# Kernel optimization log

Hardware: AMD Instinct MI355X
Metric: run time of the kernel (lower is better)

## Reference

```python
import jax, jax.numpy as jnp
import numpy as np

IN_DIM, MEM_DIM, NUM_WORDS, N_LEAVES = 300, 256, 50000, 8192


def setup_inputs() -> dict:
    key = jax.random.key(0)
    ks = jax.random.split(key, 6)
    s = 0.05
    return {
        "embs": jax.random.normal(ks[0], (N_LEAVES, IN_DIM), jnp.float32),
        "Wx": jax.random.normal(ks[1], (4 * MEM_DIM, IN_DIM), jnp.float32) * s,
        "bx": jax.random.normal(ks[2], (4 * MEM_DIM,), jnp.float32) * s,
        "Wl": jax.random.normal(ks[3], (5 * MEM_DIM, MEM_DIM), jnp.float32) * s,
        "Wr": jax.random.normal(ks[4], (5 * MEM_DIM, MEM_DIM), jnp.float32) * s,
        "emb_table": jax.random.normal(ks[5], (NUM_WORDS, IN_DIM), jnp.float32),
    }


def reference(embs, Wx, bx, Wl, Wr, emb_table):
    m = Wl.shape[1]

    # x-projection order along fused axis: [cx, ix, fx, ox]
    def proj_x(x):  # [B, in] -> [B, 4, m]
        return (x @ Wx.T + bx).reshape(x.shape[0], 4, m)

    # hidden-projection order: [u, i, lf, rf, o]
    def compose(xg, lc, lh, rc, rh):
        lg = (lh @ Wl.T).reshape(-1, 5, m)
        rg = (rh @ Wr.T).reshape(-1, 5, m)
        u = jnp.tanh(xg[:, 0] + lg[:, 0] + rg[:, 0])
        i = jax.nn.sigmoid(xg[:, 1] + lg[:, 1] + rg[:, 1])
        lf = jax.nn.sigmoid(xg[:, 2] + lg[:, 2] + rg[:, 2])  # fx shared
        rf = jax.nn.sigmoid(xg[:, 2] + lg[:, 3] + rg[:, 3])  # fx shared
        c = i * u + lf * lc + rf * rc
        o = jax.nn.sigmoid(xg[:, 3] + lg[:, 4] + rg[:, 4])
        h = o * jnp.tanh(c)
        return c, h

    # leaves: zero child states, per-leaf embedding inputs
    L = embs.shape[0]
    z = jnp.zeros((L, m), embs.dtype)
    c, h = compose(proj_x(embs), z, z, z, z)

    # internal nodes (PAD=True): input is word_embedding(num_words - 1)
    pad_xg = proj_x(emb_table[-1:])  # [1, 4, m]

    while c.shape[0] > 1:  # static shapes; 13 merge levels
        lc, rc = c[0::2], c[1::2]
        lh, rh = h[0::2], h[1::2]
        B = lc.shape[0]
        c, h = compose(jnp.broadcast_to(pad_xg, (B, 4, m)), lc, lh, rc, rh)

    return jnp.stack([c, h])  # root (c, h): [2, 1, mem_dim]
```

## Files before the change

### kernel.cpp

```cpp
#include <hip/hip_runtime.h>
#include <math.h>


#define MEM 256

typedef __attribute__((ext_vector_type(8))) short bf16x8;
typedef __attribute__((ext_vector_type(4))) float f32x4;

__device__ __forceinline__ float sigf(float x) { return 1.0f / (1.0f + __expf(-x)); }

__device__ __forceinline__ unsigned short f2b(float f) {
  unsigned int u = __float_as_uint(f);
  u = (u + 0x7FFFu + ((u >> 16) & 1u)) >> 16;
  return (unsigned short)u;
}

__device__ __forceinline__ bf16x8 c8(const float* __restrict__ p) {
  float4 f0 = *(const float4*)(p);
  float4 f1 = *(const float4*)(p + 4);
  bf16x8 r;
  r[0] = (short)f2b(f0.x); r[1] = (short)f2b(f0.y);
  r[2] = (short)f2b(f0.z); r[3] = (short)f2b(f0.w);
  r[4] = (short)f2b(f1.x); r[5] = (short)f2b(f1.y);
  r[6] = (short)f2b(f1.z); r[7] = (short)f2b(f1.w);
  return r;
}

__device__ __forceinline__ bf16x8 g8(const float* __restrict__ rp, int k0) {
  if (k0 + 8 <= 300) return c8(rp + k0);
  bf16x8 r;
#pragma unroll
  for (int j = 0; j < 8; j++) {
    int k = k0 + j;
    r[j] = (k < 300) ? (short)f2b(rp[k]) : (short)0;
  }
  return r;
}

#define NB_EB 1280
#define NB_WXF 120
__global__ __launch_bounds__(256) void k_prep1(
    const float* __restrict__ embs, const float* __restrict__ Wx,
    unsigned short* __restrict__ eb, unsigned short* __restrict__ Wxf) {
  int b = blockIdx.x, tid = threadIdx.x;
  if (b < NB_EB) {
    int idx8 = (b * 256 + tid) * 8;
    int row = idx8 / 320;
    int k0 = idx8 - row * 320;
    *(bf16x8*)(eb + idx8) = g8(embs + row * 300, k0);
  } else {
    int idx8 = ((b - NB_EB) * 256 + tid) * 8;
    int f = idx8 >> 9, rr = idx8 & 511;
    int lane = rr >> 3;
    int gate = f % 3, t = f / 3;
    int grp = t & 15, kc = t >> 4;
    int k0 = kc * 32 + ((lane >> 4) << 3);
    const int gmap[3] = {0, 1, 3};
    int n = gmap[gate] * 256 + (grp << 4) + (lane & 15);
    *(bf16x8*)(Wxf + idx8) = g8(Wx + n * 300, k0);
  }
}

#define NB_LEAF 1024
#define NB_WCF 320
__global__ __launch_bounds__(256) void k_leaf_fused(
    const unsigned short* __restrict__ eb, const unsigned short* __restrict__ Wxf,
    const float* __restrict__ bx, const float* __restrict__ Wx,
    const float* __restrict__ Wl, const float* __restrict__ Wr,
    const float* __restrict__ emb_last,
    unsigned short* __restrict__ Wcf, float* __restrict__ bias5,
    float* __restrict__ cO, unsigned short* __restrict__ hO) {
  int b = blockIdx.x, tid = threadIdx.x;
  if (b < NB_LEAF) {
    int slice = b & 7, rest = b >> 3;
    int rowblock = slice * 8 + (rest & 7);
    int grp = rest >> 3;
    int lane = tid & 63, wave = tid >> 6;
    int tb = (rowblock * 4 + wave) * 2;
    int m = lane & 15, quad = lane >> 4;

    f32x4 acc[2][3];
#pragma unroll
    for (int rt = 0; rt < 2; rt++)
#pragma unroll
      for (int g = 0; g < 3; g++) acc[rt][g] = (f32x4){0.f, 0.f, 0.f, 0.f};

    const unsigned short* ar0 = eb + (tb * 16 + m) * 320 + quad * 8;
    const unsigned short* ar1 = eb + ((tb + 1) * 16 + m) * 320 + quad * 8;
#pragma unroll
    for (int kc = 0; kc < 10; kc++) {
      const unsigned short* bp = Wxf + ((kc * 16 + grp) * 3) * 512 + lane * 8;
      bf16x8 b0 = *(const bf16x8*)(bp);
      bf16x8 b1 = *(const bf16x8*)(bp + 512);
      bf16x8 b2 = *(const bf16x8*)(bp + 1024);
      bf16x8 a0 = *(const bf16x8*)(ar0 + kc * 32);
      bf16x8 a1 = *(const bf16x8*)(ar1 + kc * 32);
      acc[0][0] = __builtin_amdgcn_mfma_f32_16x16x32_bf16(a0, b0, acc[0][0], 0, 0, 0);
      acc[0][1] = __builtin_amdgcn_mfma_f32_16x16x32_bf16(a0, b1, acc[0][1], 0, 0, 0);
      acc[0][2] = __builtin_amdgcn_mfma_f32_16x16x32_bf16(a0, b2, acc[0][2], 0, 0, 0);
      acc[1][0] = __builtin_amdgcn_mfma_f32_16x16x32_bf16(a1, b0, acc[1][0], 0, 0, 0);
      acc[1][1] = __builtin_amdgcn_mfma_f32_16x16x32_bf16(a1, b1, acc[1][1], 0, 0, 0);
      acc[1][2] = __builtin_amdgcn_mfma_f32_16x16x32_bf16(a1, b2, acc[1][2], 0, 0, 0);
    }
    int col = grp * 16 + m;
    float b0 = bx[col], b1 = bx[256 + col], b3 = bx[768 + col];
#pragma unroll
    for (int rt = 0; rt < 2; rt++) {
#pragma unroll
      for (int reg = 0; reg < 4; reg++) {
        int row = (tb + rt) * 16 + quad * 4 + reg;
        float u = tanhf(acc[rt][0][reg] + b0);
        float ig = sigf(acc[rt][1][reg] + b1);
        float o = sigf(acc[rt][2][reg] + b3);
        float c = ig * u;
        cO[row * MEM + col] = c;
        hO[row * MEM + col] = f2b(o * tanhf(c));
      }
    }
  } else if (b < NB_LEAF + NB_WCF) {
    int idx8 = ((b - NB_LEAF) * 256 + tid) * 8;
    int f = idx8 >> 9, rr = idx8 & 511;
    int lane = rr >> 3;
    int gate = f % 5, t = f / 5;
    int grp = t & 15, kc = t >> 4;
    int k0 = kc * 32 + ((lane >> 4) << 3);
    int n = gate * 256 + (grp << 4) + (lane & 15);
    const float* src = (k0 < 256) ? (Wl + n * 256 + k0) : (Wr + n * 256 + (k0 - 256));
    *(bf16x8*)(Wcf + idx8) = c8(src);
  } else {
    int g = b - (NB_LEAF + NB_WCF);
    __shared__ float er[300];
    for (int k = tid; k < 300; k += 256) er[k] = emb_last[k];
    __syncthreads();
    const int map[5] = {0, 1, 2, 2, 3};
    int wrow = map[g] * 256 + tid;
    const float* w = Wx + wrow * 300;
    float s = bx[wrow];
    for (int k = 0; k < 300; k++) s += er[k] * w[k];
    bias5[g * 256 + tid] = s;
  }
}

__global__ __launch_bounds__(256) void k_compose_rt2(
    const unsigned short* __restrict__ hprev, const float* __restrict__ cprev,
    const unsigned short* __restrict__ Wcf, const float* __restrict__ bias5,
    float* __restrict__ cO, unsigned short* __restrict__ hO, int B) {
  int bid = blockIdx.x;
  int slice = bid & 7;
  int rest = bid >> 3;
  int rowblock = slice * 4 + (rest & 3);
  int grp = rest >> 2;
  int lane = threadIdx.x & 63;
  int wave = threadIdx.x >> 6;
  int tb = (rowblock * 4 + wave) * 2;
  int m = lane & 15, quad = lane >> 4;

  f32x4 acc[2][5];
  const unsigned short* ar[2];
#pragma unroll
  for (int rt = 0; rt < 2; rt++) {
    int ra = (tb + rt) * 16 + m;
    ar[rt] = hprev + ra * 512 + quad * 8;
#pragma unroll
    for (int g = 0; g < 5; g++) acc[rt][g] = (f32x4){0.f, 0.f, 0.f, 0.f};
  }

#pragma unroll
  for (int kc = 0; kc < 16; kc++) {
    const unsigned short* bp = Wcf + ((kc * 16 + grp) * 5) * 512 + lane * 8;
    bf16x8 b0 = *(const bf16x8*)(bp);
    bf16x8 b1 = *(const bf16x8*)(bp + 512);
    bf16x8 b2 = *(const bf16x8*)(bp + 1024);
    bf16x8 b3 = *(const bf16x8*)(bp + 1536);
    bf16x8 b4 = *(const bf16x8*)(bp + 2048);
#pragma unroll
    for (int rt = 0; rt < 2; rt++) {
      bf16x8 a = *(const bf16x8*)(ar[rt] + kc * 32);
      acc[rt][0] = __builtin_amdgcn_mfma_f32_16x16x32_bf16(a, b0, acc[rt][0], 0, 0, 0);
      acc[rt][1] = __builtin_amdgcn_mfma_f32_16x16x32_bf16(a, b1, acc[rt][1], 0, 0, 0);
      acc[rt][2] = __builtin_amdgcn_mfma_f32_16x16x32_bf16(a, b2, acc[rt][2], 0, 0, 0);
      acc[rt][3] = __builtin_amdgcn_mfma_f32_16x16x32_bf16(a, b3, acc[rt][3], 0, 0, 0);
      acc[rt][4] = __builtin_amdgcn_mfma_f32_16x16x32_bf16(a, b4, acc[rt][4], 0, 0, 0);
    }
  }
  int col = grp * 16 + m;
  float b0 = bias5[col], b1 = bias5[256 + col], b2 = bias5[512 + col];
  float b3 = bias5[768 + col], b4 = bias5[1024 + col];
#pragma unroll
  for (int rt = 0; rt < 2; rt++) {
#pragma unroll
    for (int reg = 0; reg < 4; reg++) {
      int row = (tb + rt) * 16 + quad * 4 + reg;
      float u = tanhf(acc[rt][0][reg] + b0);
      float ig = sigf(acc[rt][1][reg] + b1);
      float lf = sigf(acc[rt][2][reg] + b2);
      float rf = sigf(acc[rt][3][reg] + b3);
      float o = sigf(acc[rt][4][reg] + b4);
      float lc = cprev[(2 * row) * MEM + col];
      float rc = cprev[(2 * row + 1) * MEM + col];
      float c = ig * u + lf * lc + rf * rc;
      cO[row * MEM + col] = c;
      hO[row * MEM + col] = f2b(o * tanhf(c));
    }
  }
}

__global__ __launch_bounds__(256, 4) void k_compose_ksplit(
    const unsigned short* __restrict__ hprev, const float* __restrict__ cprev,
    const unsigned short* __restrict__ Wcf, const float* __restrict__ bias5,
    float* __restrict__ cO, unsigned short* __restrict__ hO,
    float* __restrict__ hOf, int B) {
  __shared__ __align__(16) float lds[4 * 2 * 5 * 64 * 4];
  int tid = threadIdx.x;
  int lane = tid & 63, wave = tid >> 6;
  int grp = blockIdx.y;
  int tp = blockIdx.x;
  int m = lane & 15, quad = lane >> 4;
  int tiles = (B + 15) >> 4;
  const bf16x8 zz = {0, 0, 0, 0, 0, 0, 0, 0};

  f32x4 acc[2][5];
  bool act[2], ok[2];
  bf16x8 av[2][4];
#pragma unroll
  for (int t = 0; t < 2; t++) {
    int gt = 2 * tp + t;
    act[t] = (gt < tiles);
    int ra = gt * 16 + m;
    ok[t] = act[t] && (ra < B);
    const unsigned short* ar = hprev + ra * 512 + quad * 8;
#pragma unroll
    for (int kcl = 0; kcl < 4; kcl++)
      av[t][kcl] = ok[t] ? *(const bf16x8*)(ar + (wave * 4 + kcl) * 32) : zz;
#pragma unroll
    for (int q = 0; q < 5; q++) acc[t][q] = (f32x4){0.f, 0.f, 0.f, 0.f};
  }

#pragma unroll
  for (int kcl = 0; kcl < 4; kcl++) {
    int kc = wave * 4 + kcl;
    const unsigned short* bp = Wcf + ((kc * 16 + grp) * 5) * 512 + lane * 8;
    bf16x8 b0 = *(const bf16x8*)(bp);
    bf16x8 b1 = *(const bf16x8*)(bp + 512);
    bf16x8 b2 = *(const bf16x8*)(bp + 1024);
    bf16x8 b3 = *(const bf16x8*)(bp + 1536);
    bf16x8 b4 = *(const bf16x8*)(bp + 2048);
#pragma unroll
    for (int t = 0; t < 2; t++) {
      if (act[t]) {
        acc[t][0] = __builtin_amdgcn_mfma_f32_16x16x32_bf16(av[t][kcl], b0, acc[t][0], 0, 0, 0);
        acc[t][1] = __builtin_amdgcn_mfma_f32_16x16x32_bf16(av[t][kcl], b1, acc[t][1], 0, 0, 0);
        acc[t][2] = __builtin_amdgcn_mfma_f32_16x16x32_bf16(av[t][kcl], b2, acc[t][2], 0, 0, 0);
        acc[t][3] = __builtin_amdgcn_mfma_f32_16x16x32_bf16(av[t][kcl], b3, acc[t][3], 0, 0, 0);
        acc[t][4] = __builtin_amdgcn_mfma_f32_16x16x32_bf16(av[t][kcl], b4, acc[t][4], 0, 0, 0);
      }
    }
  }
#pragma unroll
  for (int t = 0; t < 2; t++)
    if (act[t])
#pragma unroll
      for (int q = 0; q < 5; q++)
        *(f32x4*)&lds[(((wave * 2 + t) * 5 + q) * 64 + lane) * 4] = acc[t][q];
  __syncthreads();

  if (wave < 2 && act[wave]) {
    int t = wave;
    int gt = 2 * tp + t;
    int col = grp * 16 + m;
    float b0 = bias5[col], b1 = bias5[256 + col], b2 = bias5[512 + col];
    float b3 = bias5[768 + col], b4 = bias5[1024 + col];
    f32x4 s[5];
#pragma unroll
    for (int q = 0; q < 5; q++) {
      s[q] = *(const f32x4*)&lds[(((0 * 2 + t) * 5 + q) * 64 + lane) * 4];
#pragma unroll
      for (int v = 1; v < 4; v++) {
        f32x4 p = *(const f32x4*)&lds[(((v * 2 + t) * 5 + q) * 64 + lane) * 4];
        s[q][0] += p[0]; s[q][1] += p[1]; s[q][2] += p[2]; s[q][3] += p[3];
      }
    }
#pragma unroll
    for (int reg = 0; reg < 4; reg++) {
      int row = gt * 16 + quad * 4 + reg;
      if (row >= B) continue;
      float u = tanhf(s[0][reg] + b0);
      float ig = sigf(s[1][reg] + b1);
      float lf = sigf(s[2][reg] + b2);
      float rf = sigf(s[3][reg] + b3);
      float o = sigf(s[4][reg] + b4);
      float lc = cprev[(2 * row) * MEM + col];
      float rc = cprev[(2 * row + 1) * MEM + col];
      float c = ig * u + lf * lc + rf * rc;
      float h = o * tanhf(c);
      cO[row * MEM + col] = c;
      hO[row * MEM + col] = f2b(h);
      if (hOf) hOf[row * MEM + col] = h;
    }
  }
}

extern "C" void kernel_launch(void* const* d_in, const int* in_sizes, int n_in,
                              void* d_out, int out_size, void* d_ws, size_t ws_size,
                              hipStream_t stream) {
  const float* embs = (const float*)d_in[0];
  const float* Wx = (const float*)d_in[1];
  const float* bx = (const float*)d_in[2];
  const float* Wl = (const float*)d_in[3];
  const float* Wr = (const float*)d_in[4];
  const float* emb_table = (const float*)d_in[5];
  float* out = (float*)d_out;

  float* ws = (float*)d_ws;
  float* cA = ws;
  float* cB = cA + 8192 * 256;
  float* bias5 = cB + 4096 * 256;
  unsigned short* hA = (unsigned short*)(bias5 + 1280);
  unsigned short* hB = hA + 8192 * 256;
  unsigned short* Wcf = hB + 4096 * 256;
  unsigned short* Wxf = Wcf + 1280 * 512;
  unsigned short* eb = Wxf + 480 * 512;

  k_prep1<<<NB_EB + NB_WXF, 256, 0, stream>>>(embs, Wx, eb, Wxf);

  k_leaf_fused<<<NB_LEAF + NB_WCF + 5, 256, 0, stream>>>(
      eb, Wxf, bx, Wx, Wl, Wr, emb_table + (in_sizes[5] - 300),
      Wcf, bias5, cA, hA);

  k_compose_rt2<<<512, 256, 0, stream>>>(hA, cA, Wcf, bias5, cB, hB, 4096);

  const float* cs = cB;
  const unsigned short* hs = hB;
  int B = 2048;
  int lvl = 1;
  while (B >= 1) {
    float* dc;
    unsigned short* dh;
    float* dhf = nullptr;
    if (B == 1) {
      dc = out;
      dh = hA;
      dhf = out + 256;
    } else if ((lvl & 1) == 0) {
      dc = cB; dh = hB;
    } else {
      dc = cA; dh = hA;
    }
    int tiles = (B + 15) / 16;
    int gx = (tiles + 1) / 2;
    k_compose_ksplit<<<dim3(gx, 16), 256, 0, stream>>>(
        hs, cs, Wcf, bias5, dc, dh, dhf, B);
    cs = dc;
    hs = dh;
    B >>= 1;
    lvl++;
  }
}
```

Measured before the change: 227.6 us.

## Fuse last ten tree levels into one persistent kernel with atomic grid barriers

The last ten compose levels (B=512 down to 1) now run in a single persistent kernel of 128 blocks instead of one launch per level. Each block keeps its 16-column slice of the hidden weights in LDS, and levels are separated by a global atomic-counter barrier. The aim is to remove launch overhead and tail latency on the small levels. It depends on all 128 blocks being co-resident and on flags being reset each call. The k-split kernel also drops its bounds checks, since it is now only launched for sizes that divide the tiles evenly.

Result: slower. 260.9 us (+14.6%).

```diff
diff --git a/kernel.cpp b/kernel.cpp
--- a/kernel.cpp
+++ b/kernel.cpp
@@ -41,8 +41,10 @@
 #define NB_WXF 120
 __global__ __launch_bounds__(256) void k_prep1(
     const float* __restrict__ embs, const float* __restrict__ Wx,
-    unsigned short* __restrict__ eb, unsigned short* __restrict__ Wxf) {
+    unsigned short* __restrict__ eb, unsigned short* __restrict__ Wxf,
+    unsigned int* __restrict__ flags) {
   int b = blockIdx.x, tid = threadIdx.x;
+  if (b == 0 && tid < 16) flags[tid] = 0u;
   if (b < NB_EB) {
     int idx8 = (b * 256 + tid) * 8;
     int row = idx8 / 320;
@@ -208,30 +210,23 @@
 __global__ __launch_bounds__(256, 4) void k_compose_ksplit(
     const unsigned short* __restrict__ hprev, const float* __restrict__ cprev,
     const unsigned short* __restrict__ Wcf, const float* __restrict__ bias5,
-    float* __restrict__ cO, unsigned short* __restrict__ hO,
-    float* __restrict__ hOf, int B) {
+    float* __restrict__ cO, unsigned short* __restrict__ hO, int B) {
   __shared__ __align__(16) float lds[4 * 2 * 5 * 64 * 4];
   int tid = threadIdx.x;
   int lane = tid & 63, wave = tid >> 6;
   int grp = blockIdx.y;
   int tp = blockIdx.x;
   int m = lane & 15, quad = lane >> 4;
-  int tiles = (B + 15) >> 4;
-  const bf16x8 zz = {0, 0, 0, 0, 0, 0, 0, 0};
 
   f32x4 acc[2][5];
-  bool act[2], ok[2];
   bf16x8 av[2][4];
 #pragma unroll
   for (int t = 0; t < 2; t++) {
-    int gt = 2 * tp + t;
-    act[t] = (gt < tiles);
-    int ra = gt * 16 + m;
-    ok[t] = act[t] && (ra < B);
+    int ra = (2 * tp + t) * 16 + m;
     const unsigned short* ar = hprev + ra * 512 + quad * 8;
 #pragma unroll
     for (int kcl = 0; kcl < 4; kcl++)
-      av[t][kcl] = ok[t] ? *(const bf16x8*)(ar + (wave * 4 + kcl) * 32) : zz;
+      av[t][kcl] = *(const bf16x8*)(ar + (wave * 4 + kcl) * 32);
 #pragma unroll
     for (int q = 0; q < 5; q++) acc[t][q] = (f32x4){0.f, 0.f, 0.f, 0.f};
   }
@@ -247,24 +242,21 @@
     bf16x8 b4 = *(const bf16x8*)(bp + 2048);
 #pragma unroll
     for (int t = 0; t < 2; t++) {
-      if (act[t]) {
-        acc[t][0] = __builtin_amdgcn_mfma_f32_16x16x32_bf16(av[t][kcl], b0, acc[t][0], 0, 0, 0);
-        acc[t][1] = __builtin_amdgcn_mfma_f32_16x16x32_bf16(av[t][kcl], b1, acc[t][1], 0, 0, 0);
-        acc[t][2] = __builtin_amdgcn_mfma_f32_16x16x32_bf16(av[t][kcl], b2, acc[t][2], 0, 0, 0);
-        acc[t][3] = __builtin_amdgcn_mfma_f32_16x16x32_bf16(av[t][kcl], b3, acc[t][3], 0, 0, 0);
-        acc[t][4] = __builtin_amdgcn_mfma_f32_16x16x32_bf16(av[t][kcl], b4, acc[t][4], 0, 0, 0);
-      }
+      acc[t][0] = __builtin_amdgcn_mfma_f32_16x16x32_bf16(av[t][kcl], b0, acc[t][0], 0, 0, 0);
+      acc[t][1] = __builtin_amdgcn_mfma_f32_16x16x32_bf16(av[t][kcl], b1, acc[t][1], 0, 0, 0);
+      acc[t][2] = __builtin_amdgcn_mfma_f32_16x16x32_bf16(av[t][kcl], b2, acc[t][2], 0, 0, 0);
+      acc[t][3] = __builtin_amdgcn_mfma_f32_16x16x32_bf16(av[t][kcl], b3, acc[t][3], 0, 0, 0);
+      acc[t][4] = __builtin_amdgcn_mfma_f32_16x16x32_bf16(av[t][kcl], b4, acc[t][4], 0, 0, 0);
     }
   }
 #pragma unroll
   for (int t = 0; t < 2; t++)
-    if (act[t])
-#pragma unroll
-      for (int q = 0; q < 5; q++)
-        *(f32x4*)&lds[(((wave * 2 + t) * 5 + q) * 64 + lane) * 4] = acc[t][q];
+#pragma unroll
+    for (int q = 0; q < 5; q++)
+      *(f32x4*)&lds[(((wave * 2 + t) * 5 + q) * 64 + lane) * 4] = acc[t][q];
   __syncthreads();
 
-  if (wave < 2 && act[wave]) {
+  if (wave < 2) {
     int t = wave;
     int gt = 2 * tp + t;
     int col = grp * 16 + m;
@@ -283,7 +275,6 @@
 #pragma unroll
     for (int reg = 0; reg < 4; reg++) {
       int row = gt * 16 + quad * 4 + reg;
-      if (row >= B) continue;
       float u = tanhf(s[0][reg] + b0);
       float ig = sigf(s[1][reg] + b1);
       float lf = sigf(s[2][reg] + b2);
@@ -292,11 +283,110 @@
       float lc = cprev[(2 * row) * MEM + col];
       float rc = cprev[(2 * row + 1) * MEM + col];
       float c = ig * u + lf * lc + rf * rc;
-      float h = o * tanhf(c);
       cO[row * MEM + col] = c;
-      hO[row * MEM + col] = f2b(h);
-      if (hOf) hOf[row * MEM + col] = h;
-    }
+      hO[row * MEM + col] = f2b(o * tanhf(c));
+    }
+  }
+}
+
+__global__ __launch_bounds__(256) void k_tail(
+    const float* __restrict__ cs0, const unsigned short* __restrict__ hs0,
+    float* __restrict__ cP0, unsigned short* __restrict__ hP0,
+    float* __restrict__ cP1, unsigned short* __restrict__ hP1,
+    const unsigned short* __restrict__ Wcf, const float* __restrict__ bias5,
+    float* __restrict__ outv, unsigned int* __restrict__ flags) {
+  __shared__ unsigned short wl[40960];
+  int bid = blockIdx.x;
+  int g = bid & 15, rp = bid >> 4;
+  int tid = threadIdx.x;
+#pragma unroll
+  for (int j = 0; j < 20; j++) {
+    int off8 = (j * 256 + tid) * 8;
+    int i = off8 >> 9, inner = off8 & 511;
+    int kc = i / 5, gate = i - kc * 5;
+    *(bf16x8*)&wl[off8] =
+        *(const bf16x8*)(Wcf + (((kc * 16 + g) * 5 + gate) << 9) + inner);
+  }
+  __syncthreads();
+  int lane = tid & 63, wave = tid >> 6;
+  int m = lane & 15, quad = lane >> 4;
+  int col = g * 16 + m;
+  float bb0 = bias5[col], bb1 = bias5[256 + col], bb2 = bias5[512 + col];
+  float bb3 = bias5[768 + col], bb4 = bias5[1024 + col];
+  const bf16x8 zz = {0, 0, 0, 0, 0, 0, 0, 0};
+
+  const float* cs = cs0;
+  const unsigned short* hs = hs0;
+  int par = 0, fi = 0;
+  for (int B = 512; B >= 1; B >>= 1) {
+    int tiles = (B + 15) >> 4;
+    float* dc = par ? cP1 : cP0;
+    unsigned short* dh = par ? hP1 : hP0;
+    int t = rp * 4 + wave;
+    if (t < tiles) {
+      f32x4 a0 = {0.f, 0.f, 0.f, 0.f}, a1 = a0, a2 = a0, a3 = a0, a4 = a0;
+      int ra = t * 16 + m;
+      bool okA = (ra < B);
+      const unsigned short* ar = hs + ra * 512 + quad * 8;
+#pragma unroll
+      for (int kh = 0; kh < 2; kh++) {
+        bf16x8 av[8];
+#pragma unroll
+        for (int j = 0; j < 8; j++)
+          av[j] = okA ? *(const bf16x8*)(ar + (kh * 8 + j) * 32) : zz;
+#pragma unroll
+        for (int j = 0; j < 8; j++) {
+          int kc = kh * 8 + j;
+          const unsigned short* wp = wl + kc * 5 * 512 + lane * 8;
+          a0 = __builtin_amdgcn_mfma_f32_16x16x32_bf16(av[j], *(const bf16x8*)(wp), a0, 0, 0, 0);
+          a1 = __builtin_amdgcn_mfma_f32_16x16x32_bf16(av[j], *(const bf16x8*)(wp + 512), a1, 0, 0, 0);
+          a2 = __builtin_amdgcn_mfma_f32_16x16x32_bf16(av[j], *(const bf16x8*)(wp + 1024), a2, 0, 0, 0);
+          a3 = __builtin_amdgcn_mfma_f32_16x16x32_bf16(av[j], *(const bf16x8*)(wp + 1536), a3, 0, 0, 0);
+          a4 = __builtin_amdgcn_mfma_f32_16x16x32_bf16(av[j], *(const bf16x8*)(wp + 2048), a4, 0, 0, 0);
+        }
+      }
+#pragma unroll
+      for (int reg = 0; reg < 4; reg++) {
+        int row = t * 16 + quad * 4 + reg;
+        if (row >= B) continue;
+        float u = tanhf(a0[reg] + bb0);
+        float ig = sigf(a1[reg] + bb1);
+        float lf = sigf(a2[reg] + bb2);
+        float rf = sigf(a3[reg] + bb3);
+        float o = sigf(a4[reg] + bb4);
+        float lc = cs[(2 * row) * MEM + col];
+        float rc = cs[(2 * row + 1) * MEM + col];
+        float c = ig * u + lf * lc + rf * rc;
+        float h = o * tanhf(c);
+        if (B == 1) {
+          outv[col] = c;
+          outv[256 + col] = h;
+        } else {
+          dc[row * MEM + col] = c;
+          dh[row * MEM + col] = f2b(h);
+        }
+      }
+    }
+    if (B == 1) break;
+    __syncthreads();
+    if (tid == 0) {
+      if (rp * 4 < tiles)
+        __hip_atomic_fetch_add(&flags[fi], 1u, __ATOMIC_RELEASE,
+                               __HIP_MEMORY_SCOPE_AGENT);
+      int arp = (tiles + 3) >> 2;
+      if (arp > 8) arp = 8;
+      unsigned expect = 16u * (unsigned)arp;
+      while (__hip_atomic_load(&flags[fi], __ATOMIC_RELAXED,
+                               __HIP_MEMORY_SCOPE_AGENT) < expect)
+        __builtin_amdgcn_s_sleep(2);
+      (void)__hip_atomic_load(&flags[fi], __ATOMIC_ACQUIRE,
+                              __HIP_MEMORY_SCOPE_AGENT);
+    }
+    __syncthreads();
+    cs = dc;
+    hs = dh;
+    par ^= 1;
+    fi++;
   }
 }
 
@@ -320,8 +410,9 @@
   unsigned short* Wcf = hB + 4096 * 256;
   unsigned short* Wxf = Wcf + 1280 * 512;
   unsigned short* eb = Wxf + 480 * 512;
-
-  k_prep1<<<NB_EB + NB_WXF, 256, 0, stream>>>(embs, Wx, eb, Wxf);
+  unsigned int* flags = (unsigned int*)(eb + 8192 * 320);
+
+  k_prep1<<<NB_EB + NB_WXF, 256, 0, stream>>>(embs, Wx, eb, Wxf, flags);
 
   k_leaf_fused<<<NB_LEAF + NB_WCF + 5, 256, 0, stream>>>(
       eb, Wxf, bx, Wx, Wl, Wr, emb_table + (in_sizes[5] - 300),
@@ -329,30 +420,11 @@
 
   k_compose_rt2<<<512, 256, 0, stream>>>(hA, cA, Wcf, bias5, cB, hB, 4096);
 
-  const float* cs = cB;
-  const unsigned short* hs = hB;
-  int B = 2048;
-  int lvl = 1;
-  while (B >= 1) {
-    float* dc;
-    unsigned short* dh;
-    float* dhf = nullptr;
-    if (B == 1) {
-      dc = out;
-      dh = hA;
-      dhf = out + 256;
-    } else if ((lvl & 1) == 0) {
-      dc = cB; dh = hB;
-    } else {
-      dc = cA; dh = hA;
-    }
-    int tiles = (B + 15) / 16;
-    int gx = (tiles + 1) / 2;
-    k_compose_ksplit<<<dim3(gx, 16), 256, 0, stream>>>(
-        hs, cs, Wcf, bias5, dc, dh, dhf, B);
-    cs = dc;
-    hs = dh;
-    B >>= 1;
-    lvl++;
-  }
-}
+  k_compose_ksplit<<<dim3(64, 16), 256, 0, stream>>>(
+      hB, cB, Wcf, bias5, cA, hA, 2048);
+
+  k_compose_ksplit<<<dim3(32, 16), 256, 0, stream>>>(
+      hA, cA, Wcf, bias5, cB, hB, 1024);
+
+  k_tail<<<128, 256, 0, stream>>>(cB, hB, cA, hA, cB, hB, Wcf, bias5, out, flags);
+}
```

## Fuse bf16 conversion into leaf GEMM via LDS and drop dedicated first-level kernel

Applied to the files above, without the earlier changes.

The separate prep kernel that converted embeddings and Wx to bf16 in global memory is removed. The leaf kernel now converts a 64-row embedding tile and its Wx column slice directly into shared memory and runs MFMA from LDS. The specialised k_compose_rt2 kernel for the first merge level is also dropped, and the k-split compose kernel handles every level, with the buffer ping-pong adjusted to match. Together this removes two kernel launches and a global bf16 round trip. In exchange, each leaf block re-converts fp32 inputs redundantly across 16 column groups and uses about 72 KB of LDS, which limits occupancy.

New measurement: 275.1 us. 1.21x slower.

```diff
diff --git a/kernel.cpp b/kernel.cpp
--- a/kernel.cpp
+++ b/kernel.cpp
@@ -37,85 +37,64 @@
   return r;
 }
 
-#define NB_EB 1280
-#define NB_WXF 120
-__global__ __launch_bounds__(256) void k_prep1(
+#define NB_LEAF 2048
+#define NB_WCF 320
+__global__ __launch_bounds__(256) void k_front(
     const float* __restrict__ embs, const float* __restrict__ Wx,
-    unsigned short* __restrict__ eb, unsigned short* __restrict__ Wxf) {
-  int b = blockIdx.x, tid = threadIdx.x;
-  if (b < NB_EB) {
-    int idx8 = (b * 256 + tid) * 8;
-    int row = idx8 / 320;
-    int k0 = idx8 - row * 320;
-    *(bf16x8*)(eb + idx8) = g8(embs + row * 300, k0);
-  } else {
-    int idx8 = ((b - NB_EB) * 256 + tid) * 8;
-    int f = idx8 >> 9, rr = idx8 & 511;
-    int lane = rr >> 3;
-    int gate = f % 3, t = f / 3;
-    int grp = t & 15, kc = t >> 4;
-    int k0 = kc * 32 + ((lane >> 4) << 3);
-    const int gmap[3] = {0, 1, 3};
-    int n = gmap[gate] * 256 + (grp << 4) + (lane & 15);
-    *(bf16x8*)(Wxf + idx8) = g8(Wx + n * 300, k0);
-  }
-}
-
-#define NB_LEAF 1024
-#define NB_WCF 320
-__global__ __launch_bounds__(256) void k_leaf_fused(
-    const unsigned short* __restrict__ eb, const unsigned short* __restrict__ Wxf,
-    const float* __restrict__ bx, const float* __restrict__ Wx,
-    const float* __restrict__ Wl, const float* __restrict__ Wr,
-    const float* __restrict__ emb_last,
+    const float* __restrict__ bx, const float* __restrict__ Wl,
+    const float* __restrict__ Wr, const float* __restrict__ emb_last,
     unsigned short* __restrict__ Wcf, float* __restrict__ bias5,
     float* __restrict__ cO, unsigned short* __restrict__ hO) {
+  __shared__ __align__(16) unsigned char smem[72704];
   int b = blockIdx.x, tid = threadIdx.x;
   if (b < NB_LEAF) {
-    int slice = b & 7, rest = b >> 3;
-    int rowblock = slice * 8 + (rest & 7);
-    int grp = rest >> 3;
+    int rb = b & 127;
+    int grp = b >> 7;
+    unsigned short* As = (unsigned short*)smem;
+    unsigned short* Bs = (unsigned short*)(smem + 41984);
+    const int gmap[3] = {0, 1, 3};
+    for (int i = tid; i < 2560; i += 256) {
+      int idx8 = i * 8;
+      int r = idx8 / 320, k0 = idx8 - r * 320;
+      *(bf16x8*)(As + r * 328 + k0) = g8(embs + (size_t)(rb * 64 + r) * 300, k0);
+    }
+    for (int i = tid; i < 1920; i += 256) {
+      int idx8 = i * 8;
+      int f = idx8 >> 9, rr = idx8 & 511;
+      int kc = f / 3, gate = f - kc * 3;
+      int ll = rr >> 3;
+      int k0 = kc * 32 + ((ll >> 4) << 3);
+      int n = gmap[gate] * 256 + grp * 16 + (ll & 15);
+      *(bf16x8*)(Bs + idx8) = g8(Wx + n * 300, k0);
+    }
+    __syncthreads();
+
     int lane = tid & 63, wave = tid >> 6;
-    int tb = (rowblock * 4 + wave) * 2;
     int m = lane & 15, quad = lane >> 4;
-
-    f32x4 acc[2][3];
-#pragma unroll
-    for (int rt = 0; rt < 2; rt++)
-#pragma unroll
-      for (int g = 0; g < 3; g++) acc[rt][g] = (f32x4){0.f, 0.f, 0.f, 0.f};
-
-    const unsigned short* ar0 = eb + (tb * 16 + m) * 320 + quad * 8;
-    const unsigned short* ar1 = eb + ((tb + 1) * 16 + m) * 320 + quad * 8;
+    f32x4 acc0 = {0.f, 0.f, 0.f, 0.f}, acc1 = acc0, acc2 = acc0;
+    const unsigned short* arow = As + (wave * 16 + m) * 328 + quad * 8;
 #pragma unroll
     for (int kc = 0; kc < 10; kc++) {
-      const unsigned short* bp = Wxf + ((kc * 16 + grp) * 3) * 512 + lane * 8;
+      bf16x8 a = *(const bf16x8*)(arow + kc * 32);
+      const unsigned short* bp = Bs + (kc * 3) * 512 + lane * 8;
       bf16x8 b0 = *(const bf16x8*)(bp);
       bf16x8 b1 = *(const bf16x8*)(bp + 512);
       bf16x8 b2 = *(const bf16x8*)(bp + 1024);
-      bf16x8 a0 = *(const bf16x8*)(ar0 + kc * 32);
-      bf16x8 a1 = *(const bf16x8*)(ar1 + kc * 32);
-      acc[0][0] = __builtin_amdgcn_mfma_f32_16x16x32_bf16(a0, b0, acc[0][0], 0, 0, 0);
-      acc[0][1] = __builtin_amdgcn_mfma_f32_16x16x32_bf16(a0, b1, acc[0][1], 0, 0, 0);
-      acc[0][2] = __builtin_amdgcn_mfma_f32_16x16x32_bf16(a0, b2, acc[0][2], 0, 0, 0);
-      acc[1][0] = __builtin_amdgcn_mfma_f32_16x16x32_bf16(a1, b0, acc[1][0], 0, 0, 0);
-      acc[1][1] = __builtin_amdgcn_mfma_f32_16x16x32_bf16(a1, b1, acc[1][1], 0, 0, 0);
-      acc[1][2] = __builtin_amdgcn_mfma_f32_16x16x32_bf16(a1, b2, acc[1][2], 0, 0, 0);
+      acc0 = __builtin_amdgcn_mfma_f32_16x16x32_bf16(a, b0, acc0, 0, 0, 0);
+      acc1 = __builtin_amdgcn_mfma_f32_16x16x32_bf16(a, b1, acc1, 0, 0, 0);
+      acc2 = __builtin_amdgcn_mfma_f32_16x16x32_bf16(a, b2, acc2, 0, 0, 0);
     }
     int col = grp * 16 + m;
     float b0 = bx[col], b1 = bx[256 + col], b3 = bx[768 + col];
 #pragma unroll
-    for (int rt = 0; rt < 2; rt++) {
-#pragma unroll
-      for (int reg = 0; reg < 4; reg++) {
-        int row = (tb + rt) * 16 + quad * 4 + reg;
-        float u = tanhf(acc[rt][0][reg] + b0);
-        float ig = sigf(acc[rt][1][reg] + b1);
-        float o = sigf(acc[rt][2][reg] + b3);
-        float c = ig * u;
-        cO[row * MEM + col] = c;
-        hO[row * MEM + col] = f2b(o * tanhf(c));
-      }
+    for (int reg = 0; reg < 4; reg++) {
+      int row = rb * 64 + wave * 16 + quad * 4 + reg;
+      float u = tanhf(acc0[reg] + b0);
+      float ig = sigf(acc1[reg] + b1);
+      float o = sigf(acc2[reg] + b3);
+      float c = ig * u;
+      cO[row * MEM + col] = c;
+      hO[row * MEM + col] = f2b(o * tanhf(c));
     }
   } else if (b < NB_LEAF + NB_WCF) {
     int idx8 = ((b - NB_LEAF) * 256 + tid) * 8;
@@ -129,7 +108,7 @@
     *(bf16x8*)(Wcf + idx8) = c8(src);
   } else {
     int g = b - (NB_LEAF + NB_WCF);
-    __shared__ float er[300];
+    float* er = (float*)smem;
     for (int k = tid; k < 300; k += 256) er[k] = emb_last[k];
     __syncthreads();
     const int map[5] = {0, 1, 2, 2, 3};
@@ -138,70 +117,6 @@
     float s = bx[wrow];
     for (int k = 0; k < 300; k++) s += er[k] * w[k];
     bias5[g * 256 + tid] = s;
-  }
-}
-
-__global__ __launch_bounds__(256) void k_compose_rt2(
-    const unsigned short* __restrict__ hprev, const float* __restrict__ cprev,
-    const unsigned short* __restrict__ Wcf, const float* __restrict__ bias5,
-    float* __restrict__ cO, unsigned short* __restrict__ hO, int B) {
-  int bid = blockIdx.x;
-  int slice = bid & 7;
-  int rest = bid >> 3;
-  int rowblock = slice * 4 + (rest & 3);
-  int grp = rest >> 2;
-  int lane = threadIdx.x & 63;
-  int wave = threadIdx.x >> 6;
-  int tb = (rowblock * 4 + wave) * 2;
-  int m = lane & 15, quad = lane >> 4;
-
-  f32x4 acc[2][5];
-  const unsigned short* ar[2];
-#pragma unroll
-  for (int rt = 0; rt < 2; rt++) {
-    int ra = (tb + rt) * 16 + m;
-    ar[rt] = hprev + ra * 512 + quad * 8;
-#pragma unroll
-    for (int g = 0; g < 5; g++) acc[rt][g] = (f32x4){0.f, 0.f, 0.f, 0.f};
-  }
-
-#pragma unroll
-  for (int kc = 0; kc < 16; kc++) {
-    const unsigned short* bp = Wcf + ((kc * 16 + grp) * 5) * 512 + lane * 8;
-    bf16x8 b0 = *(const bf16x8*)(bp);
-    bf16x8 b1 = *(const bf16x8*)(bp + 512);
-    bf16x8 b2 = *(const bf16x8*)(bp + 1024);
-    bf16x8 b3 = *(const bf16x8*)(bp + 1536);
-    bf16x8 b4 = *(const bf16x8*)(bp + 2048);
-#pragma unroll
-    for (int rt = 0; rt < 2; rt++) {
-      bf16x8 a = *(const bf16x8*)(ar[rt] + kc * 32);
-      acc[rt][0] = __builtin_amdgcn_mfma_f32_16x16x32_bf16(a, b0, acc[rt][0], 0, 0, 0);
-      acc[rt][1] = __builtin_amdgcn_mfma_f32_16x16x32_bf16(a, b1, acc[rt][1], 0, 0, 0);
-      acc[rt][2] = __builtin_amdgcn_mfma_f32_16x16x32_bf16(a, b2, acc[rt][2], 0, 0, 0);
-      acc[rt][3] = __builtin_amdgcn_mfma_f32_16x16x32_bf16(a, b3, acc[rt][3], 0, 0, 0);
-      acc[rt][4] = __builtin_amdgcn_mfma_f32_16x16x32_bf16(a, b4, acc[rt][4], 0, 0, 0);
-    }
-  }
-  int col = grp * 16 + m;
-  float b0 = bias5[col], b1 = bias5[256 + col], b2 = bias5[512 + col];
-  float b3 = bias5[768 + col], b4 = bias5[1024 + col];
-#pragma unroll
-  for (int rt = 0; rt < 2; rt++) {
-#pragma unroll
-    for (int reg = 0; reg < 4; reg++) {
-      int row = (tb + rt) * 16 + quad * 4 + reg;
-      float u = tanhf(acc[rt][0][reg] + b0);
-      float ig = sigf(acc[rt][1][reg] + b1);
-      float lf = sigf(acc[rt][2][reg] + b2);
-      float rf = sigf(acc[rt][3][reg] + b3);
-      float o = sigf(acc[rt][4][reg] + b4);
-      float lc = cprev[(2 * row) * MEM + col];
-      float rc = cprev[(2 * row + 1) * MEM + col];
-      float c = ig * u + lf * lc + rf * rc;
-      cO[row * MEM + col] = c;
-      hO[row * MEM + col] = f2b(o * tanhf(c));
-    }
   }
 }
 
@@ -228,7 +143,7 @@
     act[t] = (gt < tiles);
     int ra = gt * 16 + m;
     ok[t] = act[t] && (ra < B);
-    const unsigned short* ar = hprev + ra * 512 + quad * 8;
+    const unsigned short* ar = hprev + (size_t)ra * 512 + quad * 8;
 #pragma unroll
     for (int kcl = 0; kcl < 4; kcl++)
       av[t][kcl] = ok[t] ? *(const bf16x8*)(ar + (wave * 4 + kcl) * 32) : zz;
@@ -318,28 +233,22 @@
   unsigned short* hA = (unsigned short*)(bias5 + 1280);
   unsigned short* hB = hA + 8192 * 256;
   unsigned short* Wcf = hB + 4096 * 256;
-  unsigned short* Wxf = Wcf + 1280 * 512;
-  unsigned short* eb = Wxf + 480 * 512;
-
-  k_prep1<<<NB_EB + NB_WXF, 256, 0, stream>>>(embs, Wx, eb, Wxf);
-
-  k_leaf_fused<<<NB_LEAF + NB_WCF + 5, 256, 0, stream>>>(
-      eb, Wxf, bx, Wx, Wl, Wr, emb_table + (in_sizes[5] - 300),
+
+  k_front<<<NB_LEAF + NB_WCF + 5, 256, 0, stream>>>(
+      embs, Wx, bx, Wl, Wr, emb_table + (in_sizes[5] - 300),
       Wcf, bias5, cA, hA);
 
-  k_compose_rt2<<<512, 256, 0, stream>>>(hA, cA, Wcf, bias5, cB, hB, 4096);
-
-  const float* cs = cB;
-  const unsigned short* hs = hB;
-  int B = 2048;
-  int lvl = 1;
+  const float* cs = cA;
+  const unsigned short* hs = hA;
+  int B = 4096;
+  int lvl = 0;
   while (B >= 1) {
     float* dc;
     unsigned short* dh;
     float* dhf = nullptr;
     if (B == 1) {
       dc = out;
-      dh = hA;
+      dh = hB;
       dhf = out + 256;
     } else if ((lvl & 1) == 0) {
       dc = cB; dh = hB;
```
